# Kernel tuning notes

Hardware: AMD Instinct MI355X
Metric: run time of the kernel (lower is better)

## Reference

```python
import jax, jax.numpy as jnp
import numpy as np

DIM = 256
HEADS = 8
WS = 7
MLP_HIDDEN = int(DIM * 2.0)
LN_EPS = 1e-5


def _ln(x, g, b):
    m = x.mean(-1, keepdims=True)
    v = ((x - m) ** 2).mean(-1, keepdims=True)
    return (x - m) / jnp.sqrt(v + LN_EPS) * g + b


def setup_inputs() -> dict:
    key = jax.random.key(0)
    ks = jax.random.split(key, 6)
    B, H, W, C = 32, 56, 56, DIM
    s = lambda k, shape: jax.random.normal(k, shape, jnp.float32) * 0.02
    return {
        "x": jax.random.normal(ks[0], (B, H * W, C), jnp.float32),
        "H": H,
        "W": W,
        "norm1_g": jnp.ones((C,), jnp.float32),
        "norm1_b": jnp.zeros((C,), jnp.float32),
        "in_proj_w": s(ks[1], (3 * C, C)),
        "in_proj_b": jnp.zeros((3 * C,), jnp.float32),
        "out_proj_w": s(ks[2], (C, C)),
        "out_proj_b": jnp.zeros((C,), jnp.float32),
        "norm2_g": jnp.ones((C,), jnp.float32),
        "norm2_b": jnp.zeros((C,), jnp.float32),
        "mlp_w1": s(ks[3], (MLP_HIDDEN, C)),
        "mlp_b1": jnp.zeros((MLP_HIDDEN,), jnp.float32),
        "mlp_w2": s(ks[4], (C, MLP_HIDDEN)),
        "mlp_b2": jnp.zeros((C,), jnp.float32),
    }


def reference(x, H, W, norm1_g, norm1_b, in_proj_w, in_proj_b, out_proj_w,
              out_proj_b, norm2_g, norm2_b, mlp_w1, mlp_b1, mlp_w2, mlp_b2):
    B, N, C = x.shape
    ws = WS
    shortcut = x

    h = _ln(x, norm1_g, norm1_b).reshape(B, H, W, C)  # channels-last (equiv. math)
    pad_h = (ws - H % ws) % ws
    pad_w = (ws - W % ws) % ws
    h = jnp.pad(h, ((0, 0), (0, pad_h), (0, pad_w), (0, 0)), mode="reflect")
    Hp, Wp = H + pad_h, W + pad_w
    nh, nw = Hp // ws, Wp // ws

    # window partition -> (B*nh*nw, ws*ws, C)
    h = h.reshape(B, nh, ws, nw, ws, C).transpose(0, 1, 3, 2, 4, 5)
    h = h.reshape(B * nh * nw, ws * ws, C)

    # torch nn.MultiheadAttention (batch_first), q=k=v=h
    hd = C // HEADS
    qkv = h @ in_proj_w.T + in_proj_b               # (Bw, L, 3C)
    q, k, v = jnp.split(qkv, 3, axis=-1)
    Bw, L, _ = q.shape
    q = q.reshape(Bw, L, HEADS, hd).transpose(0, 2, 1, 3)
    k = k.reshape(Bw, L, HEADS, hd).transpose(0, 2, 1, 3)
    v = v.reshape(Bw, L, HEADS, hd).transpose(0, 2, 1, 3)
    scores = jnp.einsum("bhqd,bhkd->bhqk", q, k) / jnp.sqrt(jnp.float32(hd))
    attn = jax.nn.softmax(scores, axis=-1)
    o = jnp.einsum("bhqk,bhkd->bhqd", attn, v)
    o = o.transpose(0, 2, 1, 3).reshape(Bw, L, C)
    o = o @ out_proj_w.T + out_proj_b

    # window merge, crop padding
    o = o.reshape(B, nh, nw, ws, ws, C).transpose(0, 1, 3, 2, 4, 5)
    o = o.reshape(B, Hp, Wp, C)[:, :H, :W, :].reshape(B, N, C)

    x = shortcut + o
    h2 = _ln(x, norm2_g, norm2_b)
    h2 = jax.nn.gelu(h2 @ mlp_w1.T + mlp_b1, approximate=False) @ mlp_w2.T + mlp_b2
    return x + h2
```

## Files before the change

kernel.cpp:

```cpp
#include <hip/hip_runtime.h>
#include <hip/hip_bf16.h>
#include <math.h>

#define NTOK 3136
#define C_ 256
#define HEADS_ 8
#define HD 32
#define WS_ 7
#define L_ 49
#define NWIN 2048
#define NWH 16384
#define M_ 100352
#define MLPH 512
#define WHSZ 2048

typedef __bf16 bf16x8 __attribute__((ext_vector_type(8)));
typedef float f32x4 __attribute__((ext_vector_type(4)));

__device__ __forceinline__ unsigned short f2bf(float f) {
    union { float f; unsigned u; } v; v.f = f;
    unsigned r = v.u + 0x7fffu + ((v.u >> 16) & 1u);
    return (unsigned short)(r >> 16);
}
__device__ __forceinline__ float bf2f(unsigned short s) {
    union { unsigned u; float f; } v; v.u = ((unsigned)s) << 16;
    return v.f;
}

__device__ __forceinline__ int t2rr(int t) {
    int win = t / L_;
    int l   = t - win * L_;
    int b_  = win >> 6, wh = (win >> 3) & 7, ww = win & 7;
    int ld7 = l / WS_;
    int y   = wh * WS_ + ld7;
    int xc  = ww * WS_ + (l - ld7 * WS_);
    return b_ * NTOK + y * 56 + xc;
}

template <int NBN>
__device__ __forceinline__ void xcd_decode(int nb, int& bm, int& bn) {
    int h = blockIdx.x;
    int fid = (h & 7) * (nb >> 3) + (h >> 3);
    int bmi = fid / NBN;
    bm = bmi * 128;
    bn = (fid - bmi * NBN) * 128;
}

__global__ __launch_bounds__(256) void cvt_kernel(
    const float* __restrict__ in, unsigned short* __restrict__ out, int n)
{
    int i = blockIdx.x * 256 + threadIdx.x;
    if (i < n) out[i] = f2bf(in[i]);
}

__global__ __launch_bounds__(256) void ln_kernel(
    const float* __restrict__ x, const float* __restrict__ gamma,
    const float* __restrict__ beta, unsigned short* __restrict__ out)
{
    int wave = threadIdx.x >> 6;
    int lane = threadIdx.x & 63;
    int p = blockIdx.x * 4 + wave;
    const float* row = x + (size_t)p * C_;
    float4 v = *(const float4*)(row + lane * 4);
    float s  = v.x + v.y + v.z + v.w;
    float ss = v.x * v.x + v.y * v.y + v.z * v.z + v.w * v.w;
    #pragma unroll
    for (int m = 1; m < 64; m <<= 1) {
        s  += __shfl_xor(s, m, 64);
        ss += __shfl_xor(ss, m, 64);
    }
    float mean = s * (1.0f / C_);
    float var  = ss * (1.0f / C_) - mean * mean;
    float inv  = rsqrtf(var + 1e-5f);
    float4 gv = *(const float4*)(gamma + lane * 4);
    float4 bv = *(const float4*)(beta + lane * 4);
    int b_ = p / NTOK, n = p - b_ * NTOK;
    int y = n / 56, xc = n - y * 56;
    int win = (b_ * 8 + y / WS_) * 8 + xc / WS_;
    int l   = (y % WS_) * WS_ + (xc % WS_);
    size_t orow = (size_t)(win * L_ + l) * C_;
    unsigned short o[4];
    o[0] = f2bf((v.x - mean) * inv * gv.x + bv.x);
    o[1] = f2bf((v.y - mean) * inv * gv.y + bv.y);
    o[2] = f2bf((v.z - mean) * inv * gv.z + bv.z);
    o[3] = f2bf((v.w - mean) * inv * gv.w + bv.w);
    *(uint2*)(out + orow + lane * 4) = *(const uint2*)o;
}

#define GBM 128
#define GBN 128
#define GBK 32

__device__ __forceinline__ void gload_lds16(const void* g, void* l) {
    __builtin_amdgcn_global_load_lds(
        (const __attribute__((address_space(1))) unsigned*)g,
        (__attribute__((address_space(3))) unsigned*)l, 16, 0, 0);
}

template <int EPI, int NBN>
__global__ __launch_bounds__(256) void mgemm(
    const unsigned short* __restrict__ A, const unsigned short* __restrict__ W,
    const float* __restrict__ bias, void* __restrict__ outv,
    int M, int N, int K)
{
    __shared__ __align__(16) unsigned short As[GBM * GBK];
    __shared__ __align__(16) unsigned short Bs[GBN * GBK];

    int tid  = threadIdx.x;
    int w    = tid >> 6;
    int lane = tid & 63;
    int wr = w >> 1, wc = w & 1;
    int bm, bn;
    xcd_decode<NBN>(gridDim.x, bm, bn);
    int srow = lane >> 2;
    int scol = (lane & 3) * 8;
    int c = lane & 15, hi = lane >> 4;

    f32x4 acc[4][4] = {};

    for (int k0 = 0; k0 < K; k0 += GBK) {
        #pragma unroll
        for (int i = 0; i < 2; ++i) {
            int ra = w * 32 + i * 16;
            gload_lds16(A + (size_t)(bm + ra + srow) * K + k0 + scol, &As[ra * GBK]);
            gload_lds16(W + (size_t)(bn + ra + srow) * K + k0 + scol, &Bs[ra * GBK]);
        }
        __syncthreads();

        bf16x8 af[4], bf[4];
        #pragma unroll
        for (int mi = 0; mi < 4; ++mi)
            af[mi] = *(const bf16x8*)&As[(wr * 64 + mi * 16 + c) * GBK + hi * 8];
        #pragma unroll
        for (int ni = 0; ni < 4; ++ni)
            bf[ni] = *(const bf16x8*)&Bs[(wc * 64 + ni * 16 + c) * GBK + hi * 8];

        #pragma unroll
        for (int mi = 0; mi < 4; ++mi)
            #pragma unroll
            for (int ni = 0; ni < 4; ++ni)
                acc[mi][ni] = __builtin_amdgcn_mfma_f32_16x16x32_bf16(
                    af[mi], bf[ni], acc[mi][ni], 0, 0, 0);
        __syncthreads();
    }

    #pragma unroll
    for (int mi = 0; mi < 4; ++mi) {
        #pragma unroll
        for (int r = 0; r < 4; ++r) {
            int row = bm + wr * 64 + mi * 16 + hi * 4 + r;
            int win, l;
            if (EPI == 0) { win = row / L_; l = row - win * L_; }
            #pragma unroll
            for (int ni = 0; ni < 4; ++ni) {
                int col = bn + wc * 64 + ni * 16 + c;
                float val = acc[mi][ni][r] + bias[col];
                if (EPI == 0) {
                    int which = col >> 8;
                    int head  = (col >> 5) & 7;
                    int d     = col & 31;
                    int wh = win * HEADS_ + head;
                    size_t base = (size_t)which * ((size_t)NWH * WHSZ) + (size_t)wh * WHSZ;
                    size_t off;
                    if (which == 2)
                        off = base + (size_t)(((l >> 3) * HD + d) << 3) + (l & 7);
                    else
                        off = base + (size_t)l * HD + d;
                    ((unsigned short*)outv)[off] = f2bf(val);
                } else {
                    float g = 0.5f * val * (1.0f + erff(val * 0.70710678118654752f));
                    ((unsigned short*)outv)[(size_t)row * N + col] = f2bf(g);
                }
            }
        }
    }
}

__global__ __launch_bounds__(512) void mgemm_ln(
    const unsigned short* __restrict__ A, const unsigned short* __restrict__ W,
    const float* __restrict__ bias, const float* __restrict__ x,
    const float* __restrict__ g2, const float* __restrict__ b2,
    unsigned short* __restrict__ x1_out, unsigned short* __restrict__ ln_out)
{
    __shared__ __align__(16) unsigned short As[128 * 32];
    __shared__ __align__(16) unsigned short Bs[256 * 32];
    __shared__ __align__(16) unsigned short X1s[128][256];

    int tid  = threadIdx.x;
    int w    = tid >> 6;
    int lane = tid & 63;
    int wr = w >> 2, wc = w & 3;
    int bm = blockIdx.x * 128;
    int srow = lane >> 2;
    int scol = (lane & 3) * 8;
    int c = lane & 15, hi = lane >> 4;

    f32x4 acc[4][4] = {};

    for (int k0 = 0; k0 < 256; k0 += 32) {
        gload_lds16(A + (size_t)(bm + w * 16 + srow) * 256 + k0 + scol,
                    &As[(w * 16) * 32]);
        #pragma unroll
        for (int i = 0; i < 2; ++i) {
            int ra = w * 32 + i * 16;
            gload_lds16(W + (size_t)(ra + srow) * 256 + k0 + scol, &Bs[ra * 32]);
        }
        __syncthreads();

        bf16x8 af[4], bf[4];
        #pragma unroll
        for (int mi = 0; mi < 4; ++mi)
            af[mi] = *(const bf16x8*)&As[(wr * 64 + mi * 16 + c) * 32 + hi * 8];
        #pragma unroll
        for (int ni = 0; ni < 4; ++ni)
            bf[ni] = *(const bf16x8*)&Bs[(wc * 64 + ni * 16 + c) * 32 + hi * 8];

        #pragma unroll
        for (int mi = 0; mi < 4; ++mi)
            #pragma unroll
            for (int ni = 0; ni < 4; ++ni)
                acc[mi][ni] = __builtin_amdgcn_mfma_f32_16x16x32_bf16(
                    af[mi], bf[ni], acc[mi][ni], 0, 0, 0);
        __syncthreads();
    }

    #pragma unroll
    for (int mi = 0; mi < 4; ++mi) {
        #pragma unroll
        for (int ni = 0; ni < 4; ++ni) {
            int colb = wc * 64 + ni * 16 + c;
            float bv = bias[colb];
            #pragma unroll
            for (int r = 0; r < 4; ++r)
                X1s[wr * 64 + mi * 16 + hi * 4 + r][colb] = f2bf(acc[mi][ni][r] + bv);
        }
    }
    __syncthreads();

    float4 gv = *(const float4*)(g2 + lane * 4);
    float4 bv2 = *(const float4*)(b2 + lane * 4);
    #pragma unroll 2
    for (int i = 0; i < 16; ++i) {
        int tl = w * 16 + i;
        int t = bm + tl;
        int rr = t2rr(t);
        float4 xv = *(const float4*)(x + (size_t)rr * C_ + lane * 4);
        uint2 ov = *(const uint2*)&X1s[tl][lane * 4];
        float x0 = xv.x + bf2f(ov.x & 0xffff);
        float x1 = xv.y + bf2f(ov.x >> 16);
        float x2 = xv.z + bf2f(ov.y & 0xffff);
        float x3 = xv.w + bf2f(ov.y >> 16);
        float s  = x0 + x1 + x2 + x3;
        float ss = x0 * x0 + x1 * x1 + x2 * x2 + x3 * x3;
        #pragma unroll
        for (int m = 1; m < 64; m <<= 1) {
            s  += __shfl_xor(s, m, 64);
            ss += __shfl_xor(ss, m, 64);
        }
        float mean = s * (1.0f / C_);
        float var  = ss * (1.0f / C_) - mean * mean;
        float inv  = rsqrtf(var + 1e-5f);
        uint2 xw, lw;
        xw.x = (unsigned)f2bf(x0) | ((unsigned)f2bf(x1) << 16);
        xw.y = (unsigned)f2bf(x2) | ((unsigned)f2bf(x3) << 16);
        float l0 = (x0 - mean) * inv * gv.x + bv2.x;
        float l1 = (x1 - mean) * inv * gv.y + bv2.y;
        float l2 = (x2 - mean) * inv * gv.z + bv2.z;
        float l3 = (x3 - mean) * inv * gv.w + bv2.w;
        lw.x = (unsigned)f2bf(l0) | ((unsigned)f2bf(l1) << 16);
        lw.y = (unsigned)f2bf(l2) | ((unsigned)f2bf(l3) << 16);
        *(uint2*)(x1_out + (size_t)t * C_ + lane * 4) = xw;
        *(uint2*)(ln_out + (size_t)t * C_ + lane * 4) = lw;
    }
}

__global__ __launch_bounds__(256) void mgemm_out(
    const unsigned short* __restrict__ A, const unsigned short* __restrict__ W,
    const float* __restrict__ bias, const unsigned short* __restrict__ x1,
    float* __restrict__ dout)
{
    __shared__ __align__(16) unsigned short lds_pool[8192];
    unsigned short* As = lds_pool;
    unsigned short* Bs = lds_pool + 4096;
    float* stage = (float*)lds_pool;

    int tid  = threadIdx.x;
    int w    = tid >> 6;
    int lane = tid & 63;
    int wr = w >> 1, wc = w & 1;
    int bm, bn;
    xcd_decode<2>(gridDim.x, bm, bn);
    int srow = lane >> 2;
    int scol = (lane & 3) * 8;
    int c = lane & 15, hi = lane >> 4;

    f32x4 acc[4][4] = {};

    for (int k0 = 0; k0 < 512; k0 += 32) {
        #pragma unroll
        for (int i = 0; i < 2; ++i) {
            int ra = w * 32 + i * 16;
            gload_lds16(A + (size_t)(bm + ra + srow) * 512 + k0 + scol, &As[ra * 32]);
            gload_lds16(W + (size_t)(bn + ra + srow) * 512 + k0 + scol, &Bs[ra * 32]);
        }
        __syncthreads();

        bf16x8 af[4], bf[4];
        #pragma unroll
        for (int mi = 0; mi < 4; ++mi)
            af[mi] = *(const bf16x8*)&As[(wr * 64 + mi * 16 + c) * 32 + hi * 8];
        #pragma unroll
        for (int ni = 0; ni < 4; ++ni)
            bf[ni] = *(const bf16x8*)&Bs[(wc * 64 + ni * 16 + c) * 32 + hi * 8];

        #pragma unroll
        for (int mi = 0; mi < 4; ++mi)
            #pragma unroll
            for (int ni = 0; ni < 4; ++ni)
                acc[mi][ni] = __builtin_amdgcn_mfma_f32_16x16x32_bf16(
                    af[mi], bf[ni], acc[mi][ni], 0, 0, 0);
        __syncthreads();
    }

    #pragma unroll
    for (int c2 = 0; c2 < 4; ++c2) {
        if (wr == (c2 >> 1)) {
            int mi0 = (c2 & 1) * 2;
            #pragma unroll
            for (int mm = 0; mm < 2; ++mm) {
                #pragma unroll
                for (int ni = 0; ni < 4; ++ni) {
                    int colb = wc * 64 + ni * 16 + c;
                    float bv = bias[bn + colb];
                    #pragma unroll
                    for (int r = 0; r < 4; ++r)
                        stage[(mm * 16 + hi * 4 + r) * 128 + colb] =
                            acc[mi0 + mm][ni][r] + bv;
                }
            }
        }
        __syncthreads();
        #pragma unroll
        for (int i = 0; i < 4; ++i) {
            int lr = i * 8 + (tid >> 5);
            int t = bm + c2 * 32 + lr;
            int rr = t2rr(t);
            int col4 = (tid & 31) * 4;
            float4 v = *(const float4*)&stage[lr * 128 + col4];
            uint2 rv = *(const uint2*)&x1[(size_t)t * C_ + bn + col4];
            v.x += bf2f(rv.x & 0xffff);
            v.y += bf2f(rv.x >> 16);
            v.z += bf2f(rv.y & 0xffff);
            v.w += bf2f(rv.y >> 16);
            *(float4*)&dout[(size_t)rr * C_ + bn + col4] = v;
        }
        __syncthreads();
    }
}

__global__ __launch_bounds__(256) void mattn(
    const unsigned short* __restrict__ qkv, unsigned short* __restrict__ o_win)
{
    __shared__ __align__(16) unsigned short P_lds[4][64][72];
    int wave = threadIdx.x >> 6, lane = threadIdx.x & 63;
    int c = lane & 15, hi = lane >> 4;
    int wh = blockIdx.x * 4 + wave;
    int win = wh >> 3, head = wh & 7;
    const unsigned short* qb = qkv + (size_t)wh * WHSZ;
    const unsigned short* kb = qb + (size_t)NWH * WHSZ;
    const unsigned short* vb = kb + (size_t)NWH * WHSZ;

    bf16x8 af[4], bk[4];
    #pragma unroll
    for (int mi = 0; mi < 4; ++mi)
        af[mi] = *(const bf16x8*)(qb + (mi * 16 + c) * HD + hi * 8);
    #pragma unroll
    for (int ni = 0; ni < 4; ++ni)
        bk[ni] = *(const bf16x8*)(kb + (ni * 16 + c) * HD + hi * 8);

    f32x4 sacc[4][4] = {};
    #pragma unroll
    for (int mi = 0; mi < 4; ++mi)
        #pragma unroll
        for (int ni = 0; ni < 4; ++ni)
            sacc[mi][ni] = __builtin_amdgcn_mfma_f32_16x16x32_bf16(
                af[mi], bk[ni], sacc[mi][ni], 0, 0, 0);

    const float scale = 0.17677669529663687f;
    float inv_[4][4];
    #pragma unroll
    for (int mi = 0; mi < 4; ++mi) {
        #pragma unroll
        for (int r = 0; r < 4; ++r) {
            float sv[4];
            float m = -1e30f;
            #pragma unroll
            for (int ni = 0; ni < 4; ++ni) {
                float v = sacc[mi][ni][r] * scale;
                v = (ni * 16 + c < L_) ? v : -1e30f;
                sv[ni] = v;
                m = fmaxf(m, v);
            }
            #pragma unroll
            for (int msk = 1; msk < 16; msk <<= 1)
                m = fmaxf(m, __shfl_xor(m, msk, 64));
            float sum = 0.f;
            unsigned short pb[4];
            #pragma unroll
            for (int ni = 0; ni < 4; ++ni) {
                float p = __expf(sv[ni] - m);
                sum += p;
                pb[ni] = f2bf(p);
            }
            #pragma unroll
            for (int msk = 1; msk < 16; msk <<= 1)
                sum += __shfl_xor(sum, msk, 64);
            inv_[mi][r] = 1.0f / sum;
            int q = mi * 16 + hi * 4 + r;
            #pragma unroll
            for (int ni = 0; ni < 4; ++ni)
                P_lds[wave][q][ni * 16 + c] = pb[ni];
        }
    }

    f32x4 oacc[4][2] = {};
    #pragma unroll
    for (int ks = 0; ks < 2; ++ks) {
        bf16x8 pa[4], bv[2];
        #pragma unroll
        for (int mi = 0; mi < 4; ++mi)
            pa[mi] = *(const bf16x8*)&P_lds[wave][mi * 16 + c][ks * 32 + hi * 8];
        #pragma unroll
        for (int ni = 0; ni < 2; ++ni)
            bv[ni] = *(const bf16x8*)(vb + ((ks * 4 + hi) * HD + ni * 16 + c) * 8);
        #pragma unroll
        for (int mi = 0; mi < 4; ++mi)
            #pragma unroll
            for (int ni = 0; ni < 2; ++ni)
                oacc[mi][ni] = __builtin_amdgcn_mfma_f32_16x16x32_bf16(
                    pa[mi], bv[ni], oacc[mi][ni], 0, 0, 0);
    }

    #pragma unroll
    for (int mi = 0; mi < 4; ++mi) {
        #pragma unroll
        for (int r = 0; r < 4; ++r) {
            int q = mi * 16 + hi * 4 + r;
            if (q < L_) {
                size_t rowoff = ((size_t)(win * L_ + q)) * C_ + head * HD;
                float iv = inv_[mi][r];
                #pragma unroll
                for (int ni = 0; ni < 2; ++ni)
                    o_win[rowoff + ni * 16 + c] = f2bf(oacc[mi][ni][r] * iv);
            }
        }
    }
}

extern "C" void kernel_launch(void* const* d_in, const int* in_sizes, int n_in,
                              void* d_out, int out_size, void* d_ws, size_t ws_size,
                              hipStream_t stream)
{
    (void)in_sizes; (void)n_in; (void)out_size; (void)ws_size;
    const float* x    = (const float*)d_in[0];
    const float* n1g  = (const float*)d_in[3];
    const float* n1b  = (const float*)d_in[4];
    const float* wqkv = (const float*)d_in[5];
    const float* bqkv = (const float*)d_in[6];
    const float* wout = (const float*)d_in[7];
    const float* bout = (const float*)d_in[8];
    const float* n2g  = (const float*)d_in[9];
    const float* n2b  = (const float*)d_in[10];
    const float* w1   = (const float*)d_in[11];
    const float* b1   = (const float*)d_in[12];
    const float* w2   = (const float*)d_in[13];
    const float* b2   = (const float*)d_in[14];
    float* out = (float*)d_out;

    unsigned short* bufA_bf = (unsigned short*)d_ws;
    unsigned short* qkv_bf  = bufA_bf + (size_t)M_ * C_;
    unsigned short* x1_bf   = qkv_bf + (size_t)3 * NWH * WHSZ;
    unsigned short* ln2_bf  = x1_bf + (size_t)M_ * C_;
    unsigned short* wqkv_bf = ln2_bf + (size_t)M_ * C_;
    unsigned short* wout_bf = wqkv_bf + 768 * 256;
    unsigned short* w1_bf   = wout_bf + 256 * 256;
    unsigned short* w2_bf   = w1_bf + 512 * 256;

    cvt_kernel<<<(768 * 256 + 255) / 256, 256, 0, stream>>>(wqkv, wqkv_bf, 768 * 256);
    cvt_kernel<<<(256 * 256 + 255) / 256, 256, 0, stream>>>(wout, wout_bf, 256 * 256);
    cvt_kernel<<<(512 * 256 + 255) / 256, 256, 0, stream>>>(w1, w1_bf, 512 * 256);
    cvt_kernel<<<(256 * 512 + 255) / 256, 256, 0, stream>>>(w2, w2_bf, 256 * 512);

    ln_kernel<<<M_ / 4, 256, 0, stream>>>(x, n1g, n1b, bufA_bf);

    mgemm<0, 6><<<(M_ / GBM) * 6, 256, 0, stream>>>(
        bufA_bf, wqkv_bf, bqkv, qkv_bf, M_, 3 * C_, C_);

    mattn<<<NWH / 4, 256, 0, stream>>>(qkv_bf, bufA_bf);

    mgemm_ln<<<M_ / 128, 512, 0, stream>>>(
        bufA_bf, wout_bf, bout, x, n2g, n2b, x1_bf, ln2_bf);

    mgemm<2, 4><<<(M_ / GBM) * 4, 256, 0, stream>>>(
        ln2_bf, w1_bf, b1, qkv_bf, M_, MLPH, C_);

    mgemm_out<<<(M_ / 128) * 2, 256, 0, stream>>>(
        qkv_bf, w2_bf, b2, x1_bf, out);
}
```

Measured before the change: 423.4 us.

## Pad windows to 64 tokens, stage GEMM epilogues through LDS, swizzle LDS, tanh-GELU

The LN1 output is laid out with each window padded to 64 rows, so the QKV GEMM emits whole-window planes for Q, K and V. Its results are staged through LDS and written as coalesced 16-byte stores instead of scattered 2-byte stores. All GEMM LDS tiles get an XOR swizzle to reduce bank conflicts. The MLP GELU switches from exact erf to a tanh/sigmoid approximation, which can change numerics. Padding adds about 30% extra rows of QKV GEMM work, and workspace buffers are aliased across stages.

New measurement: 447.2 us. +5.6%, slower.

```diff
diff --git a/kernel.cpp b/kernel.cpp
--- a/kernel.cpp
+++ b/kernel.cpp
@@ -11,8 +11,9 @@
 #define NWIN 2048
 #define NWH 16384
 #define M_ 100352
+#define MP 131072
+#define PLANE 33554432
 #define MLPH 512
-#define WHSZ 2048
 
 typedef __bf16 bf16x8 __attribute__((ext_vector_type(8)));
 typedef float f32x4 __attribute__((ext_vector_type(4)));
@@ -60,7 +61,18 @@
     int wave = threadIdx.x >> 6;
     int lane = threadIdx.x & 63;
     int p = blockIdx.x * 4 + wave;
-    const float* row = x + (size_t)p * C_;
+    int win = p >> 6, l = p & 63;
+    if (l >= L_) {
+        uint2 z; z.x = 0; z.y = 0;
+        *(uint2*)(out + (size_t)p * C_ + lane * 4) = z;
+        return;
+    }
+    int b_ = win >> 6, wh = (win >> 3) & 7, ww = win & 7;
+    int ld7 = l / WS_;
+    int y   = wh * WS_ + ld7;
+    int xc  = ww * WS_ + (l - ld7 * WS_);
+    int rr  = b_ * NTOK + y * 56 + xc;
+    const float* row = x + (size_t)rr * C_;
     float4 v = *(const float4*)(row + lane * 4);
     float s  = v.x + v.y + v.z + v.w;
     float ss = v.x * v.x + v.y * v.y + v.z * v.z + v.w * v.w;
@@ -74,21 +86,14 @@
     float inv  = rsqrtf(var + 1e-5f);
     float4 gv = *(const float4*)(gamma + lane * 4);
     float4 bv = *(const float4*)(beta + lane * 4);
-    int b_ = p / NTOK, n = p - b_ * NTOK;
-    int y = n / 56, xc = n - y * 56;
-    int win = (b_ * 8 + y / WS_) * 8 + xc / WS_;
-    int l   = (y % WS_) * WS_ + (xc % WS_);
-    size_t orow = (size_t)(win * L_ + l) * C_;
     unsigned short o[4];
     o[0] = f2bf((v.x - mean) * inv * gv.x + bv.x);
     o[1] = f2bf((v.y - mean) * inv * gv.y + bv.y);
     o[2] = f2bf((v.z - mean) * inv * gv.z + bv.z);
     o[3] = f2bf((v.w - mean) * inv * gv.w + bv.w);
-    *(uint2*)(out + orow + lane * 4) = *(const uint2*)o;
-}
-
-#define GBM 128
-#define GBN 128
+    *(uint2*)(out + (size_t)p * C_ + lane * 4) = *(const uint2*)o;
+}
+
 #define GBK 32
 
 __device__ __forceinline__ void gload_lds16(const void* g, void* l) {
@@ -97,44 +102,46 @@
         (__attribute__((address_space(3))) unsigned*)l, 16, 0, 0);
 }
 
-template <int EPI, int NBN>
-__global__ __launch_bounds__(256) void mgemm(
+#define TSS 136
+
+__global__ __launch_bounds__(256) void mgemm_qkv(
     const unsigned short* __restrict__ A, const unsigned short* __restrict__ W,
-    const float* __restrict__ bias, void* __restrict__ outv,
-    int M, int N, int K)
-{
-    __shared__ __align__(16) unsigned short As[GBM * GBK];
-    __shared__ __align__(16) unsigned short Bs[GBN * GBK];
+    const float* __restrict__ bias, unsigned short* __restrict__ Qp,
+    unsigned short* __restrict__ Kp, unsigned short* __restrict__ Vp)
+{
+    __shared__ __align__(16) unsigned short pool[64 * TSS];
+    unsigned short* As = pool;
+    unsigned short* Bs = pool + 4096;
+    unsigned short* Ts = pool;
 
     int tid  = threadIdx.x;
     int w    = tid >> 6;
     int lane = tid & 63;
     int wr = w >> 1, wc = w & 1;
     int bm, bn;
-    xcd_decode<NBN>(gridDim.x, bm, bn);
+    xcd_decode<6>(gridDim.x, bm, bn);
     int srow = lane >> 2;
-    int scol = (lane & 3) * 8;
+    int scol = ((lane & 3) ^ ((lane >> 3) & 3)) * 8;
     int c = lane & 15, hi = lane >> 4;
+    int hs = (hi ^ ((c >> 1) & 3)) * 8;
 
     f32x4 acc[4][4] = {};
 
-    for (int k0 = 0; k0 < K; k0 += GBK) {
+    for (int k0 = 0; k0 < 256; k0 += GBK) {
         #pragma unroll
         for (int i = 0; i < 2; ++i) {
             int ra = w * 32 + i * 16;
-            gload_lds16(A + (size_t)(bm + ra + srow) * K + k0 + scol, &As[ra * GBK]);
-            gload_lds16(W + (size_t)(bn + ra + srow) * K + k0 + scol, &Bs[ra * GBK]);
-        }
-        __syncthreads();
-
+            gload_lds16(A + (size_t)(bm + ra + srow) * 256 + k0 + scol, As + ra * GBK);
+            gload_lds16(W + (size_t)(bn + ra + srow) * 256 + k0 + scol, Bs + ra * GBK);
+        }
+        __syncthreads();
         bf16x8 af[4], bf[4];
         #pragma unroll
         for (int mi = 0; mi < 4; ++mi)
-            af[mi] = *(const bf16x8*)&As[(wr * 64 + mi * 16 + c) * GBK + hi * 8];
+            af[mi] = *(const bf16x8*)&As[(wr * 64 + mi * 16 + c) * GBK + hs];
         #pragma unroll
         for (int ni = 0; ni < 4; ++ni)
-            bf[ni] = *(const bf16x8*)&Bs[(wc * 64 + ni * 16 + c) * GBK + hi * 8];
-
+            bf[ni] = *(const bf16x8*)&Bs[(wc * 64 + ni * 16 + c) * GBK + hs];
         #pragma unroll
         for (int mi = 0; mi < 4; ++mi)
             #pragma unroll
@@ -144,37 +151,129 @@
         __syncthreads();
     }
 
-    #pragma unroll
-    for (int mi = 0; mi < 4; ++mi) {
-        #pragma unroll
-        for (int r = 0; r < 4; ++r) {
-            int row = bm + wr * 64 + mi * 16 + hi * 4 + r;
-            int win, l;
-            if (EPI == 0) { win = row / L_; l = row - win * L_; }
-            #pragma unroll
-            for (int ni = 0; ni < 4; ++ni) {
-                int col = bn + wc * 64 + ni * 16 + c;
-                float val = acc[mi][ni][r] + bias[col];
-                if (EPI == 0) {
-                    int which = col >> 8;
-                    int head  = (col >> 5) & 7;
-                    int d     = col & 31;
-                    int wh = win * HEADS_ + head;
-                    size_t base = (size_t)which * ((size_t)NWH * WHSZ) + (size_t)wh * WHSZ;
-                    size_t off;
-                    if (which == 2)
-                        off = base + (size_t)(((l >> 3) * HD + d) << 3) + (l & 7);
-                    else
-                        off = base + (size_t)l * HD + d;
-                    ((unsigned short*)outv)[off] = f2bf(val);
-                } else {
-                    float g = 0.5f * val * (1.0f + erff(val * 0.70710678118654752f));
-                    ((unsigned short*)outv)[(size_t)row * N + col] = f2bf(g);
+    int which  = bn >> 8;
+    int bn_off = bn & 255;
+    unsigned short* plane = (which == 0) ? Qp : (which == 1) ? Kp : Vp;
+
+    #pragma unroll
+    for (int ch = 0; ch < 2; ++ch) {
+        if (wr == ch) {
+            #pragma unroll
+            for (int mi = 0; mi < 4; ++mi)
+                #pragma unroll
+                for (int ni = 0; ni < 4; ++ni) {
+                    int colb = wc * 64 + ni * 16 + c;
+                    float bv = bias[bn + colb];
+                    #pragma unroll
+                    for (int r = 0; r < 4; ++r)
+                        Ts[(mi * 16 + hi * 4 + r) * TSS + colb] =
+                            f2bf(acc[mi][ni][r] + bv);
                 }
+        }
+        __syncthreads();
+        int win = (bm >> 6) + ch;
+        if (which < 2) {
+            #pragma unroll
+            for (int it = 0; it < 4; ++it) {
+                int id = it * 256 + tid;
+                int row = id >> 4, cx = (id & 15) * 8;
+                uint4 v = *(const uint4*)&Ts[row * TSS + cx];
+                *(uint4*)&plane[(size_t)win * 16384 + (size_t)row * 256 + bn_off + cx] = v;
             }
-        }
-    }
-}
+        } else {
+            #pragma unroll
+            for (int it = 0; it < 4; ++it) {
+                int id = it * 256 + tid;
+                int kb = id >> 7, colloc = id & 127;
+                union { unsigned short s[8]; uint4 v; } u;
+                #pragma unroll
+                for (int kj = 0; kj < 8; ++kj)
+                    u.s[kj] = Ts[(kb * 8 + kj) * TSS + colloc];
+                *(uint4*)&plane[(size_t)win * 16384 +
+                                (size_t)(kb * 256 + bn_off + colloc) * 8] = u.v;
+            }
+        }
+        __syncthreads();
+    }
+}
+
+__global__ __launch_bounds__(256) void mgemm_g(
+    const unsigned short* __restrict__ A, const unsigned short* __restrict__ W,
+    const float* __restrict__ bias, unsigned short* __restrict__ outp)
+{
+    __shared__ __align__(16) unsigned short pool[64 * TSS];
+    unsigned short* As = pool;
+    unsigned short* Bs = pool + 4096;
+    unsigned short* Ts = pool;
+
+    int tid  = threadIdx.x;
+    int w    = tid >> 6;
+    int lane = tid & 63;
+    int wr = w >> 1, wc = w & 1;
+    int bm, bn;
+    xcd_decode<4>(gridDim.x, bm, bn);
+    int srow = lane >> 2;
+    int scol = ((lane & 3) ^ ((lane >> 3) & 3)) * 8;
+    int c = lane & 15, hi = lane >> 4;
+    int hs = (hi ^ ((c >> 1) & 3)) * 8;
+
+    f32x4 acc[4][4] = {};
+
+    for (int k0 = 0; k0 < 256; k0 += GBK) {
+        #pragma unroll
+        for (int i = 0; i < 2; ++i) {
+            int ra = w * 32 + i * 16;
+            gload_lds16(A + (size_t)(bm + ra + srow) * 256 + k0 + scol, As + ra * GBK);
+            gload_lds16(W + (size_t)(bn + ra + srow) * 256 + k0 + scol, Bs + ra * GBK);
+        }
+        __syncthreads();
+        bf16x8 af[4], bf[4];
+        #pragma unroll
+        for (int mi = 0; mi < 4; ++mi)
+            af[mi] = *(const bf16x8*)&As[(wr * 64 + mi * 16 + c) * GBK + hs];
+        #pragma unroll
+        for (int ni = 0; ni < 4; ++ni)
+            bf[ni] = *(const bf16x8*)&Bs[(wc * 64 + ni * 16 + c) * GBK + hs];
+        #pragma unroll
+        for (int mi = 0; mi < 4; ++mi)
+            #pragma unroll
+            for (int ni = 0; ni < 4; ++ni)
+                acc[mi][ni] = __builtin_amdgcn_mfma_f32_16x16x32_bf16(
+                    af[mi], bf[ni], acc[mi][ni], 0, 0, 0);
+        __syncthreads();
+    }
+
+    #pragma unroll
+    for (int ch = 0; ch < 2; ++ch) {
+        if (wr == ch) {
+            #pragma unroll
+            for (int mi = 0; mi < 4; ++mi)
+                #pragma unroll
+                for (int ni = 0; ni < 4; ++ni) {
+                    int colb = wc * 64 + ni * 16 + c;
+                    float bv = bias[bn + colb];
+                    #pragma unroll
+                    for (int r = 0; r < 4; ++r) {
+                        float v = acc[mi][ni][r] + bv;
+                        float a = 1.5957691216f * (v + 0.044715f * v * v * v);
+                        float g = v / (1.0f + __expf(-a));
+                        Ts[(mi * 16 + hi * 4 + r) * TSS + colb] = f2bf(g);
+                    }
+                }
+        }
+        __syncthreads();
+        #pragma unroll
+        for (int it = 0; it < 4; ++it) {
+            int id = it * 256 + tid;
+            int row = id >> 4, cx = (id & 15) * 8;
+            uint4 v = *(const uint4*)&Ts[row * TSS + cx];
+            *(uint4*)&outp[(size_t)(bm + ch * 64 + row) * MLPH + bn + cx] = v;
+        }
+        __syncthreads();
+    }
+}
+
+#define XS 260
 
 __global__ __launch_bounds__(512) void mgemm_ln(
     const unsigned short* __restrict__ A, const unsigned short* __restrict__ W,
@@ -182,9 +281,9 @@
     const float* __restrict__ g2, const float* __restrict__ b2,
     unsigned short* __restrict__ x1_out, unsigned short* __restrict__ ln_out)
 {
-    __shared__ __align__(16) unsigned short As[128 * 32];
-    __shared__ __align__(16) unsigned short Bs[256 * 32];
-    __shared__ __align__(16) unsigned short X1s[128][256];
+    __shared__ __align__(16) unsigned short pool[128 * XS];
+    unsigned short* As = pool;
+    unsigned short* Bs = pool + 4096;
 
     int tid  = threadIdx.x;
     int w    = tid >> 6;
@@ -192,29 +291,28 @@
     int wr = w >> 2, wc = w & 3;
     int bm = blockIdx.x * 128;
     int srow = lane >> 2;
-    int scol = (lane & 3) * 8;
+    int scol = ((lane & 3) ^ ((lane >> 3) & 3)) * 8;
     int c = lane & 15, hi = lane >> 4;
+    int hs = (hi ^ ((c >> 1) & 3)) * 8;
 
     f32x4 acc[4][4] = {};
 
-    for (int k0 = 0; k0 < 256; k0 += 32) {
+    for (int k0 = 0; k0 < 256; k0 += GBK) {
         gload_lds16(A + (size_t)(bm + w * 16 + srow) * 256 + k0 + scol,
-                    &As[(w * 16) * 32]);
+                    As + (w * 16) * GBK);
         #pragma unroll
         for (int i = 0; i < 2; ++i) {
             int ra = w * 32 + i * 16;
-            gload_lds16(W + (size_t)(ra + srow) * 256 + k0 + scol, &Bs[ra * 32]);
-        }
-        __syncthreads();
-
+            gload_lds16(W + (size_t)(ra + srow) * 256 + k0 + scol, Bs + ra * GBK);
+        }
+        __syncthreads();
         bf16x8 af[4], bf[4];
         #pragma unroll
         for (int mi = 0; mi < 4; ++mi)
-            af[mi] = *(const bf16x8*)&As[(wr * 64 + mi * 16 + c) * 32 + hi * 8];
+            af[mi] = *(const bf16x8*)&As[(wr * 64 + mi * 16 + c) * GBK + hs];
         #pragma unroll
         for (int ni = 0; ni < 4; ++ni)
-            bf[ni] = *(const bf16x8*)&Bs[(wc * 64 + ni * 16 + c) * 32 + hi * 8];
-
+            bf[ni] = *(const bf16x8*)&Bs[(wc * 64 + ni * 16 + c) * GBK + hs];
         #pragma unroll
         for (int mi = 0; mi < 4; ++mi)
             #pragma unroll
@@ -232,12 +330,13 @@
             float bv = bias[colb];
             #pragma unroll
             for (int r = 0; r < 4; ++r)
-                X1s[wr * 64 + mi * 16 + hi * 4 + r][colb] = f2bf(acc[mi][ni][r] + bv);
+                pool[(wr * 64 + mi * 16 + hi * 4 + r) * XS + colb] =
+                    f2bf(acc[mi][ni][r] + bv);
         }
     }
     __syncthreads();
 
-    float4 gv = *(const float4*)(g2 + lane * 4);
+    float4 gv  = *(const float4*)(g2 + lane * 4);
     float4 bv2 = *(const float4*)(b2 + lane * 4);
     #pragma unroll 2
     for (int i = 0; i < 16; ++i) {
@@ -245,7 +344,7 @@
         int t = bm + tl;
         int rr = t2rr(t);
         float4 xv = *(const float4*)(x + (size_t)rr * C_ + lane * 4);
-        uint2 ov = *(const uint2*)&X1s[tl][lane * 4];
+        uint2 ov = *(const uint2*)&pool[tl * XS + lane * 4];
         float x0 = xv.x + bf2f(ov.x & 0xffff);
         float x1 = xv.y + bf2f(ov.x >> 16);
         float x2 = xv.z + bf2f(ov.y & 0xffff);
@@ -279,10 +378,10 @@
     const float* __restrict__ bias, const unsigned short* __restrict__ x1,
     float* __restrict__ dout)
 {
-    __shared__ __align__(16) unsigned short lds_pool[8192];
-    unsigned short* As = lds_pool;
-    unsigned short* Bs = lds_pool + 4096;
-    float* stage = (float*)lds_pool;
+    __shared__ __align__(16) unsigned short pool[8704];
+    unsigned short* As = pool;
+    unsigned short* Bs = pool + 4096;
+    float* stg = (float*)pool;
 
     int tid  = threadIdx.x;
     int w    = tid >> 6;
@@ -291,28 +390,27 @@
     int bm, bn;
     xcd_decode<2>(gridDim.x, bm, bn);
     int srow = lane >> 2;
-    int scol = (lane & 3) * 8;
+    int scol = ((lane & 3) ^ ((lane >> 3) & 3)) * 8;
     int c = lane & 15, hi = lane >> 4;
+    int hs = (hi ^ ((c >> 1) & 3)) * 8;
 
     f32x4 acc[4][4] = {};
 
-    for (int k0 = 0; k0 < 512; k0 += 32) {
+    for (int k0 = 0; k0 < 512; k0 += GBK) {
         #pragma unroll
         for (int i = 0; i < 2; ++i) {
             int ra = w * 32 + i * 16;
-            gload_lds16(A + (size_t)(bm + ra + srow) * 512 + k0 + scol, &As[ra * 32]);
-            gload_lds16(W + (size_t)(bn + ra + srow) * 512 + k0 + scol, &Bs[ra * 32]);
-        }
-        __syncthreads();
-
+            gload_lds16(A + (size_t)(bm + ra + srow) * 512 + k0 + scol, As + ra * GBK);
+            gload_lds16(W + (size_t)(bn + ra + srow) * 512 + k0 + scol, Bs + ra * GBK);
+        }
+        __syncthreads();
         bf16x8 af[4], bf[4];
         #pragma unroll
         for (int mi = 0; mi < 4; ++mi)
-            af[mi] = *(const bf16x8*)&As[(wr * 64 + mi * 16 + c) * 32 + hi * 8];
+            af[mi] = *(const bf16x8*)&As[(wr * 64 + mi * 16 + c) * GBK + hs];
         #pragma unroll
         for (int ni = 0; ni < 4; ++ni)
-            bf[ni] = *(const bf16x8*)&Bs[(wc * 64 + ni * 16 + c) * 32 + hi * 8];
-
+            bf[ni] = *(const bf16x8*)&Bs[(wc * 64 + ni * 16 + c) * GBK + hs];
         #pragma unroll
         for (int mi = 0; mi < 4; ++mi)
             #pragma unroll
@@ -334,7 +432,7 @@
                     float bv = bias[bn + colb];
                     #pragma unroll
                     for (int r = 0; r < 4; ++r)
-                        stage[(mm * 16 + hi * 4 + r) * 128 + colb] =
+                        stg[(mm * 16 + hi * 4 + r) * 132 + colb] =
                             acc[mi0 + mm][ni][r] + bv;
                 }
             }
@@ -346,7 +444,7 @@
             int t = bm + c2 * 32 + lr;
             int rr = t2rr(t);
             int col4 = (tid & 31) * 4;
-            float4 v = *(const float4*)&stage[lr * 128 + col4];
+            float4 v = *(const float4*)&stg[lr * 132 + col4];
             uint2 rv = *(const uint2*)&x1[(size_t)t * C_ + bn + col4];
             v.x += bf2f(rv.x & 0xffff);
             v.y += bf2f(rv.x >> 16);
@@ -359,24 +457,25 @@
 }
 
 __global__ __launch_bounds__(256) void mattn(
-    const unsigned short* __restrict__ qkv, unsigned short* __restrict__ o_win)
+    const unsigned short* __restrict__ Qp, const unsigned short* __restrict__ Kp,
+    const unsigned short* __restrict__ Vp, unsigned short* __restrict__ o_win)
 {
     __shared__ __align__(16) unsigned short P_lds[4][64][72];
     int wave = threadIdx.x >> 6, lane = threadIdx.x & 63;
     int c = lane & 15, hi = lane >> 4;
     int wh = blockIdx.x * 4 + wave;
     int win = wh >> 3, head = wh & 7;
-    const unsigned short* qb = qkv + (size_t)wh * WHSZ;
-    const unsigned short* kb = qb + (size_t)NWH * WHSZ;
-    const unsigned short* vb = kb + (size_t)NWH * WHSZ;
+    const unsigned short* qb = Qp + (size_t)win * 16384 + head * HD;
+    const unsigned short* kb = Kp + (size_t)win * 16384 + head * HD;
+    const unsigned short* vb = Vp + (size_t)win * 16384 + head * HD * 8;
 
     bf16x8 af[4], bk[4];
     #pragma unroll
     for (int mi = 0; mi < 4; ++mi)
-        af[mi] = *(const bf16x8*)(qb + (mi * 16 + c) * HD + hi * 8);
+        af[mi] = *(const bf16x8*)(qb + (size_t)(mi * 16 + c) * 256 + hi * 8);
     #pragma unroll
     for (int ni = 0; ni < 4; ++ni)
-        bk[ni] = *(const bf16x8*)(kb + (ni * 16 + c) * HD + hi * 8);
+        bk[ni] = *(const bf16x8*)(kb + (size_t)(ni * 16 + c) * 256 + hi * 8);
 
     f32x4 sacc[4][4] = {};
     #pragma unroll
@@ -432,7 +531,7 @@
             pa[mi] = *(const bf16x8*)&P_lds[wave][mi * 16 + c][ks * 32 + hi * 8];
         #pragma unroll
         for (int ni = 0; ni < 2; ++ni)
-            bv[ni] = *(const bf16x8*)(vb + ((ks * 4 + hi) * HD + ni * 16 + c) * 8);
+            bv[ni] = *(const bf16x8*)(vb + (size_t)((ks * 4 + hi) * 256 + ni * 16 + c) * 8);
         #pragma unroll
         for (int mi = 0; mi < 4; ++mi)
             #pragma unroll
@@ -477,33 +576,35 @@
     const float* b2   = (const float*)d_in[14];
     float* out = (float*)d_out;
 
-    unsigned short* bufA_bf = (unsigned short*)d_ws;
-    unsigned short* qkv_bf  = bufA_bf + (size_t)M_ * C_;
-    unsigned short* x1_bf   = qkv_bf + (size_t)3 * NWH * WHSZ;
-    unsigned short* ln2_bf  = x1_bf + (size_t)M_ * C_;
-    unsigned short* wqkv_bf = ln2_bf + (size_t)M_ * C_;
+    unsigned short* lnq   = (unsigned short*)d_ws;
+    unsigned short* Qp    = lnq + (size_t)MP * C_;
+    unsigned short* Kp    = Qp + (size_t)PLANE;
+    unsigned short* Vp    = Kp + (size_t)PLANE;
+    unsigned short* o_win = Vp + (size_t)PLANE;
+    unsigned short* wqkv_bf = o_win + (size_t)M_ * C_;
     unsigned short* wout_bf = wqkv_bf + 768 * 256;
     unsigned short* w1_bf   = wout_bf + 256 * 256;
     unsigned short* w2_bf   = w1_bf + 512 * 256;
+    unsigned short* x1_bf  = lnq;
+    unsigned short* ln2_bf = Vp;
+    unsigned short* gelu   = Qp;
 
     cvt_kernel<<<(768 * 256 + 255) / 256, 256, 0, stream>>>(wqkv, wqkv_bf, 768 * 256);
     cvt_kernel<<<(256 * 256 + 255) / 256, 256, 0, stream>>>(wout, wout_bf, 256 * 256);
     cvt_kernel<<<(512 * 256 + 255) / 256, 256, 0, stream>>>(w1, w1_bf, 512 * 256);
     cvt_kernel<<<(256 * 512 + 255) / 256, 256, 0, stream>>>(w2, w2_bf, 256 * 512);
 
-    ln_kernel<<<M_ / 4, 256, 0, stream>>>(x, n1g, n1b, bufA_bf);
-
-    mgemm<0, 6><<<(M_ / GBM) * 6, 256, 0, stream>>>(
-        bufA_bf, wqkv_bf, bqkv, qkv_bf, M_, 3 * C_, C_);
-
-    mattn<<<NWH / 4, 256, 0, stream>>>(qkv_bf, bufA_bf);
+    ln_kernel<<<MP / 4, 256, 0, stream>>>(x, n1g, n1b, lnq);
+
+    mgemm_qkv<<<(MP / 128) * 6, 256, 0, stream>>>(
+        lnq, wqkv_bf, bqkv, Qp, Kp, Vp);
+
+    mattn<<<NWH / 4, 256, 0, stream>>>(Qp, Kp, Vp, o_win);
 
     mgemm_ln<<<M_ / 128, 512, 0, stream>>>(
-        bufA_bf, wout_bf, bout, x, n2g, n2b, x1_bf, ln2_bf);
-
-    mgemm<2, 4><<<(M_ / GBM) * 4, 256, 0, stream>>>(
-        ln2_bf, w1_bf, b1, qkv_bf, M_, MLPH, C_);
-
-    mgemm_out<<<(M_ / 128) * 2, 256, 0, stream>>>(
-        qkv_bf, w2_bf, b2, x1_bf, out);
-}
+        o_win, wout_bf, bout, x, n2g, n2b, x1_bf, ln2_bf);
+
+    mgemm_g<<<(M_ / 128) * 4, 256, 0, stream>>>(ln2_bf, w1_bf, b1, gelu);
+
+    mgemm_out<<<(M_ / 128) * 2, 256, 0, stream>>>(gelu, w2_bf, b2, x1_bf, out);
+}
```
